# Performance work log

Measured on AMD Instinct MI355X. Metric: run time of the kernel, lower is better.

## Reference

```python
import jax, jax.numpy as jnp
import numpy as np
import math

B, S, D, H = 16, 1024, 512, 8
DK = D // H  # 64
EPS_T = 1e-06   # temperature epsilon
LN_EPS = 1e-05  # torch LayerNorm default


def gelu_tanh(x):
    return 0.5 * x * (1 + jnp.tanh(math.sqrt(2.0 / math.pi) * (x + 0.044715 * x ** 3)))


def layer_norm(x, g, b):
    mu = jnp.mean(x, axis=-1, keepdims=True)
    var = jnp.mean((x - mu) ** 2, axis=-1, keepdims=True)
    return (x - mu) * jax.lax.rsqrt(var + LN_EPS) * g + b


def setup_inputs() -> dict:
    key = jax.random.key(0)
    ks = jax.random.split(key, 12)
    std_qkv = np.sqrt(2.0 / (D + D)).astype(np.float32)
    inp = {
        "Q": jax.random.normal(ks[0], (B, S, D), jnp.float32),
        "K": jax.random.normal(ks[1], (B, S, D), jnp.float32),
        "V": jax.random.normal(ks[2], (B, S, D), jnp.float32),
        "mask": jnp.zeros((B, S), dtype=bool),  # no padding
        "W_q": jax.random.normal(ks[3], (D, D), jnp.float32) * std_qkv,
        "W_k": jax.random.normal(ks[4], (D, D), jnp.float32) * std_qkv,
        "W_v": jax.random.normal(ks[5], (D, D), jnp.float32) * std_qkv,
        "W_o": jax.random.normal(ks[6], (D, D), jnp.float32) * std_qkv,
        "lin1_w": jax.random.normal(ks[7], (D, D), jnp.float32) * std_qkv,  # stored [in,out]
        "lin1_b": jnp.zeros((D,), jnp.float32),
        "lin2_w": jax.random.normal(ks[8], (D, D), jnp.float32) * std_qkv,
        "lin2_b": jnp.zeros((D,), jnp.float32),
        "ln_g": jnp.ones((D,), jnp.float32),
        "ln_b": jnp.zeros((D,), jnp.float32),
    }
    return inp


def reference(Q, K, V, mask, W_q, W_k, W_v, W_o, lin1_w, lin1_b, lin2_w, lin2_b, ln_g, ln_b):
    b, q_len, _ = Q.shape
    # projections -> (b, h, s, d_k)
    Qh = (Q @ W_q).reshape(b, q_len, H, DK).transpose(0, 2, 1, 3)
    Kh = (K @ W_k).reshape(b, q_len, H, DK).transpose(0, 2, 1, 3)
    Vh = (V @ W_v).reshape(b, q_len, H, DK).transpose(0, 2, 1, 3)

    temperature = DK ** 0.5
    scores = jnp.einsum("bhqd,bhkd->bhqk", Qh, Kh) / (temperature + EPS_T)

    # mask: causal triu(diag=1) OR pad mask broadcast along k (as in original)
    causal = jnp.triu(jnp.ones((q_len, q_len), dtype=bool), k=1)  # (q,k)
    pad = mask[:, None, :, None]                                  # (b,1,q,1)
    mask_ = causal[None, None, :, :] | pad                        # (b,1,q,k)
    scores = jnp.where(mask_, -1e10, scores)

    attn = jax.nn.softmax(scores, axis=-1)
    ctx = jnp.einsum("bhqk,bhkd->bhqd", attn, Vh)
    ctx = ctx.transpose(0, 2, 1, 3).reshape(b, q_len, H * DK)
    v_att = ctx @ W_o  # dropout = identity (eval)

    out = layer_norm(Q + v_att, ln_g, ln_b)
    ffn = gelu_tanh(out @ lin1_w + lin1_b) @ lin2_w + lin2_b
    out = layer_norm(ffn + out, ln_g, ln_b)
    return out
```

## Files before the change

### kernel.cpp

```cpp
#include <hip/hip_runtime.h>
#include <cstdint>

using f32x4  = __attribute__((ext_vector_type(4))) float;
using f16x8  = __attribute__((ext_vector_type(8))) _Float16;
using f16x4  = __attribute__((ext_vector_type(4))) _Float16;
using f16x2  = __attribute__((ext_vector_type(2))) _Float16;

#define DEV static __device__ __forceinline__

DEV _Float16 f2h(float f) { return (_Float16)f; }

#if __has_builtin(__builtin_amdgcn_exp2f)
#define EXP2(x) __builtin_amdgcn_exp2f(x)
#else
#define EXP2(x) __expf((x) * 0.6931471805599453f)
#endif

DEV void gl2lds16(const void* g, void* l) {
  __builtin_amdgcn_global_load_lds(
      (__attribute__((address_space(1))) void*)(uintptr_t)g,
      (__attribute__((address_space(3))) void*)(uint32_t)(uintptr_t)l,
      16, 0, 0);
}

DEV f16x2 pack2(float a, float b) {
  return __builtin_bit_cast(f16x2, __builtin_amdgcn_cvt_pkrtz(a, b));
}

template <int MODE>
__global__ __launch_bounds__(256, 2) void gemm_k(
    const _Float16* __restrict__ A, const _Float16* __restrict__ Bt,
    const float* __restrict__ bias, _Float16* __restrict__ outB) {
  __shared__ _Float16 As[2][8192];
  __shared__ _Float16 Bs[2][8192];
  const int tid = threadIdx.x;
  const int lane = tid & 63, wv = tid >> 6;
  const int quad = lane >> 4, l16 = lane & 15;
  const int wm = wv & 1, wn = wv >> 1;

  const int bid = blockIdx.x;
  const int c8 = bid & 7, t8 = bid >> 3;
  const int nt = t8 & 3, gg = t8 >> 2;
  const int mz = gg * 8 + c8;
  const int m0 = (mz & 127) * 128;
  const int zz = (MODE == 0) ? (mz >> 7) : 0;
  const int n0 = nt * 128;

  const size_t zo = (size_t)zz * 8388608;
  const _Float16* Az = A + zo + (size_t)m0 * 512;
  const _Float16* Bz = Bt + (size_t)zz * 262144 + (size_t)n0 * 512;
  _Float16* Oz = outB + zo;

  f32x4 acc[4][4] = {};

  int aoff[4];
#pragma unroll
  for (int j = 0; j < 4; j++) {
    int e = j * 256 + tid;
    int r = e >> 3, c = e & 7;
    aoff[j] = r * 512 + (c ^ (r & 7)) * 8;
  }

  auto stage = [&](int kt, int pb) {
    const _Float16* Ab = Az + kt * 64;
    const _Float16* Bb = Bz + kt * 64;
#pragma unroll
    for (int j = 0; j < 4; j++)
      gl2lds16(Ab + aoff[j], &As[pb][(j * 256 + tid) * 8]);
#pragma unroll
    for (int j = 0; j < 4; j++)
      gl2lds16(Bb + aoff[j], &Bs[pb][(j * 256 + tid) * 8]);
  };

  stage(0, 0);
  __syncthreads();

  for (int kt = 0; kt < 8; kt++) {
    const int pb = kt & 1;
    if (kt < 7) stage(kt + 1, pb ^ 1);
    f16x8 af[2][4], bf[2][4];
#pragma unroll
    for (int kc = 0; kc < 2; kc++) {
#pragma unroll
      for (int i = 0; i < 4; i++) {
        int row = wm * 64 + i * 16 + l16;
        int q = (kc * 4 + quad) ^ (row & 7);
        af[kc][i] = *(const f16x8*)&As[pb][row * 64 + q * 8];
      }
#pragma unroll
      for (int j = 0; j < 4; j++) {
        int row = wn * 64 + j * 16 + l16;
        int q = (kc * 4 + quad) ^ (row & 7);
        bf[kc][j] = *(const f16x8*)&Bs[pb][row * 64 + q * 8];
      }
    }
#pragma unroll
    for (int kc = 0; kc < 2; kc++)
#pragma unroll
      for (int i = 0; i < 4; i++)
#pragma unroll
        for (int j = 0; j < 4; j++)
          acc[i][j] = __builtin_amdgcn_mfma_f32_16x16x32_f16(
              af[kc][i], bf[kc][j], acc[i][j], 0, 0, 0);
    __syncthreads();
  }

#pragma unroll
  for (int i = 0; i < 4; i++) {
#pragma unroll
    for (int j = 0; j < 4; j++) {
      const size_t col = n0 + wn * 64 + j * 16 + l16;
#pragma unroll
      for (int r = 0; r < 4; r++) {
        const size_t row = m0 + wm * 64 + i * 16 + quad * 4 + r;
        float v = acc[i][j][r];
        if (MODE == 0) {
          size_t b = row >> 10, s = row & 1023, h = col >> 6, d = col & 63;
          Oz[(((b * 8 + h) << 10) + s) * 64 + d] = f2h(v);
        } else if (MODE == 1) {
          Oz[row * 512 + col] = f2h(v);
        } else if (MODE == 2) {
          float x = v + bias[col];
          float u = 0.7978845608028654f * (x + 0.044715f * x * x * x);
          float t = __expf(2.f * u);
          float th = 1.f - 2.f / (t + 1.f);
          Oz[row * 512 + col] = f2h(0.5f * x * (1.f + th));
        } else {
          Oz[row * 512 + col] = f2h(v + bias[col]);
        }
      }
    }
  }
}

__global__ __launch_bounds__(256, 2) void attn_k(
    const _Float16* __restrict__ Qh, const _Float16* __restrict__ Kh,
    const _Float16* __restrict__ Vt, _Float16* __restrict__ ctx) {
  __shared__ _Float16 lds[16384];

  const int bid = blockIdx.x;
  const int pair = bid >> 7;
  const int bh = bid & 127;

  const _Float16* Qp = Qh + (size_t)bh * 65536;
  const _Float16* Kp = Kh + (size_t)bh * 65536;
  const _Float16* Vp = Vt + (size_t)bh * 65536;

  const int tid = threadIdx.x, lane = tid & 63, wv = tid >> 6;
  const int quad = lane >> 4, l16 = lane & 15;
  const int s7 = l16 & 7;
  const int b = bh >> 3, h = bh & 7;

  const int lin0 = 2 * wv * 64 + lane, lin1 = (2 * wv + 1) * 64 + lane;
  const int rK0 = lin0 >> 3, chK0 = (lane & 7) ^ (rK0 & 7);
  const int rK1 = lin1 >> 3, chK1 = (lane & 7) ^ (rK1 & 7);

  auto stage = [&](int kt, int pb) {
    _Float16* Kb = lds + pb * 4096;
    _Float16* Vb = lds + 8192 + pb * 4096;
    gl2lds16(Kp + (size_t)(kt * 64 + rK0) * 64 + chK0 * 8, Kb + lin0 * 8);
    gl2lds16(Kp + (size_t)(kt * 64 + rK1) * 64 + chK1 * 8, Kb + lin1 * 8);
    gl2lds16(Vp + (size_t)rK0 * 1024 + kt * 64 + chK0 * 8, Vb + lin0 * 8);
    gl2lds16(Vp + (size_t)rK1 * 1024 + kt * 64 + chK1 * 8, Vb + lin1 * 8);
  };

  const _Float16 qsc = f2h((1.0f / (8.0f + 1e-6f)) * 1.4426950408889634f);
  const f16x2 ones = {(_Float16)1.0f, (_Float16)1.0f};
  const float NEGM = -12.0f;

  for (int half = 0; half < 2; half++) {
    const int qblk = half ? (7 - pair) : pair;
    const int q0 = qblk * 128;
    const int ktmax = 2 * qblk + 1;
    const int wdiag = 2 * qblk + (wv >> 1);

    f16x8 bq[2][2];
#pragma unroll
    for (int qs = 0; qs < 2; qs++)
#pragma unroll
      for (int kc = 0; kc < 2; kc++) {
        f16x8 t = *(const f16x8*)&Qp[(size_t)(q0 + wv * 32 + qs * 16 + l16) *
                                         64 +
                                     kc * 32 + quad * 8];
#pragma unroll
        for (int r = 0; r < 8; r++) t[r] = t[r] * qsc;
        bq[qs][kc] = t;
      }
    int qg[2];
    qg[0] = q0 + wv * 32 + l16;
    qg[1] = qg[0] + 16;

    f32x4 ot[4][2] = {};
    float lrun[2] = {0.f, 0.f};

    stage(0, 0);
    __syncthreads();

    for (int kt = 0; kt <= ktmax; kt++) {
      if (kt < ktmax) stage(kt + 1, (kt + 1) & 1);

      if (kt <= wdiag) {
        const _Float16* Ks = lds + (kt & 1) * 4096;
        const _Float16* Vs = lds + 8192 + (kt & 1) * 4096;

        f32x4 sa[4][2];
#pragma unroll
        for (int ms = 0; ms < 4; ms++)
#pragma unroll
          for (int qs = 0; qs < 2; qs++)
            sa[ms][qs] = f32x4{NEGM, NEGM, NEGM, NEGM};

#pragma unroll
        for (int ms = 0; ms < 4; ms++) {
          const int row = ms * 16 + l16;
          const int sl0 = quad ^ s7;
          f16x8 ka0 = *(const f16x8*)&Ks[row * 64 + sl0 * 8];
          f16x8 ka1 = *(const f16x8*)&Ks[row * 64 + (sl0 ^ 4) * 8];
#pragma unroll
          for (int qs = 0; qs < 2; qs++) {
            sa[ms][qs] = __builtin_amdgcn_mfma_f32_16x16x32_f16(
                ka0, bq[qs][0], sa[ms][qs], 0, 0, 0);
            sa[ms][qs] = __builtin_amdgcn_mfma_f32_16x16x32_f16(
                ka1, bq[qs][1], sa[ms][qs], 0, 0, 0);
          }
        }

        if (kt == wdiag) {
#pragma unroll
          for (int ms = 0; ms < 4; ms++)
#pragma unroll
            for (int qs = 0; qs < 2; qs++)
#pragma unroll
              for (int r = 0; r < 4; r++) {
                int kg = kt * 64 + ms * 16 + quad * 4 + r;
                if (kg > qg[qs]) sa[ms][qs][r] = -3.0e38f;
              }
        }

        f16x4 pf[4][2];
#pragma unroll
        for (int ms = 0; ms < 4; ms++)
#pragma unroll
          for (int qs = 0; qs < 2; qs++) {
            float e0 = EXP2(sa[ms][qs][0]);
            float e1 = EXP2(sa[ms][qs][1]);
            float e2 = EXP2(sa[ms][qs][2]);
            float e3 = EXP2(sa[ms][qs][3]);
            f16x2 lo = pack2(e0, e1);
            f16x2 hi = pack2(e2, e3);
            lrun[qs] = __builtin_amdgcn_fdot2(lo, ones, lrun[qs], false);
            lrun[qs] = __builtin_amdgcn_fdot2(hi, ones, lrun[qs], false);
            f16x4 pk;
            pk[0] = lo[0]; pk[1] = lo[1]; pk[2] = hi[0]; pk[3] = hi[1];
            pf[ms][qs] = pk;
          }

#pragma unroll
        for (int ms = 0; ms < 4; ms++) {
          const int ch0 = (ms * 2 + (quad >> 1)) ^ s7;
#pragma unroll
          for (int ds = 0; ds < 4; ds++) {
            const int row = ds * 16 + l16;
            f16x4 vf =
                *(const f16x4*)&Vs[row * 64 + ch0 * 8 + (quad & 1) * 4];
#pragma unroll
            for (int qs = 0; qs < 2; qs++)
              ot[ds][qs] = __builtin_amdgcn_mfma_f32_16x16x16f16(
                  vf, pf[ms][qs], ot[ds][qs], 0, 0, 0);
          }
        }
      }
      __syncthreads();
    }

    float rinv[2];
#pragma unroll
    for (int qs = 0; qs < 2; qs++) {
      lrun[qs] += __shfl_xor(lrun[qs], 16, 64);
      lrun[qs] += __shfl_xor(lrun[qs], 32, 64);
      rinv[qs] = 1.0f / lrun[qs];
    }

    _Float16* Ol = lds + wv * 2176;
#pragma unroll
    for (int ds = 0; ds < 4; ds++)
#pragma unroll
      for (int qs = 0; qs < 2; qs++) {
        f16x4 pk;
#pragma unroll
        for (int r = 0; r < 4; r++) pk[r] = f2h(ot[ds][qs][r] * rinv[qs]);
        *(f16x4*)&Ol[(qs * 16 + l16) * 68 + ds * 16 + quad * 4] = pk;
      }
    __syncthreads();

#pragma unroll
    for (int rep = 0; rep < 4; rep++) {
      const int qq = rep * 8 + (lane >> 3);
      const int dc = lane & 7;
      f16x4 a = *(const f16x4*)&Ol[qq * 68 + dc * 8];
      f16x4 c = *(const f16x4*)&Ol[qq * 68 + dc * 8 + 4];
      f16x8 v;
      v[0] = a[0]; v[1] = a[1]; v[2] = a[2]; v[3] = a[3];
      v[4] = c[0]; v[5] = c[1]; v[6] = c[2]; v[7] = c[3];
      size_t row = (size_t)b * 1024 + q0 + wv * 32 + qq;
      *(f16x8*)&ctx[row * 512 + h * 64 + dc * 8] = v;
    }
    __syncthreads();
  }
}

__global__ void cast3_k(const float* __restrict__ Q, const float* __restrict__ K,
                        const float* __restrict__ V, _Float16* __restrict__ Qb,
                        _Float16* __restrict__ Kb, _Float16* __restrict__ Vb) {
  size_t i = (size_t)blockIdx.x * 256 + threadIdx.x;
  float4 q = ((const float4*)Q)[i];
  float4 k = ((const float4*)K)[i];
  float4 v = ((const float4*)V)[i];
  f16x4 o;
  o[0] = f2h(q.x); o[1] = f2h(q.y); o[2] = f2h(q.z); o[3] = f2h(q.w);
  ((f16x4*)Qb)[i] = o;
  o[0] = f2h(k.x); o[1] = f2h(k.y); o[2] = f2h(k.z); o[3] = f2h(k.w);
  ((f16x4*)Kb)[i] = o;
  o[0] = f2h(v.x); o[1] = f2h(v.y); o[2] = f2h(v.z); o[3] = f2h(v.w);
  ((f16x4*)Vb)[i] = o;
}

__global__ void wtrans_k(const float* W0, const float* W1, const float* W2,
                         const float* W3, const float* W4, const float* W5,
                         _Float16* dst) {
  __shared__ float t[32][33];
  const int z = blockIdx.z;
  const float* src = (z == 0) ? W0 : (z == 1) ? W1 : (z == 2) ? W2
                    : (z == 3) ? W3 : (z == 4) ? W4 : W5;
  _Float16* out = dst + (size_t)z * 262144;
  const int k0 = blockIdx.x * 32, n0 = blockIdx.y * 32;
  const int x = threadIdx.x, y = threadIdx.y;
  for (int j = y; j < 32; j += 8) t[j][x] = src[(size_t)(k0 + j) * 512 + n0 + x];
  __syncthreads();
  for (int j = y; j < 32; j += 8)
    out[(size_t)(n0 + j) * 512 + k0 + x] = f2h(t[x][j]);
}

__global__ void vtrans_k(const _Float16* __restrict__ Vh,
                         _Float16* __restrict__ Vt) {
  __shared__ _Float16 t[32][33];
  const int bh = blockIdx.z;
  const int s0 = blockIdx.x * 32, d0 = blockIdx.y * 32;
  const _Float16* src = Vh + (size_t)bh * 65536;
  _Float16* dst = Vt + (size_t)bh * 65536;
  const int x = threadIdx.x, y = threadIdx.y;
  for (int j = y; j < 32; j += 8) t[j][x] = src[(size_t)(s0 + j) * 64 + d0 + x];
  __syncthreads();
  for (int j = y; j < 32; j += 8)
    dst[(size_t)(d0 + j) * 1024 + s0 + x] = t[x][j];
}

template <bool F32OUT>
__global__ __launch_bounds__(128) void ln_k(
    const _Float16* __restrict__ X0, const _Float16* __restrict__ X1,
    const float* __restrict__ g, const float* __restrict__ bb,
    float* __restrict__ outF, _Float16* __restrict__ outB) {
  __shared__ float sh[4];
  const int row = blockIdx.x, t = threadIdx.x;
  const size_t base4 = (size_t)row * 128 + t;
  f16x4 a = ((const f16x4*)X0)[base4];
  f16x4 c = ((const f16x4*)X1)[base4];
  float x0 = (float)a[0] + (float)c[0];
  float x1 = (float)a[1] + (float)c[1];
  float x2 = (float)a[2] + (float)c[2];
  float x3 = (float)a[3] + (float)c[3];
  float s = x0 + x1 + x2 + x3;
  float ss = x0 * x0 + x1 * x1 + x2 * x2 + x3 * x3;
#pragma unroll
  for (int off = 1; off <= 32; off <<= 1) {
    s += __shfl_xor(s, off, 64);
    ss += __shfl_xor(ss, off, 64);
  }
  if ((t & 63) == 0) { sh[(t >> 6) * 2] = s; sh[(t >> 6) * 2 + 1] = ss; }
  __syncthreads();
  s = sh[0] + sh[2];
  ss = sh[1] + sh[3];
  const float mu = s * (1.f / 512.f);
  const float var = ss * (1.f / 512.f) - mu * mu;
  const float rstd = rsqrtf(var + 1e-5f);
  float4 gv = *(const float4*)(g + t * 4);
  float4 bv = *(const float4*)(bb + t * 4);
  float y0 = (x0 - mu) * rstd * gv.x + bv.x;
  float y1 = (x1 - mu) * rstd * gv.y + bv.y;
  float y2 = (x2 - mu) * rstd * gv.z + bv.z;
  float y3 = (x3 - mu) * rstd * gv.w + bv.w;
  if (F32OUT) {
    float4 o; o.x = y0; o.y = y1; o.z = y2; o.w = y3;
    *(float4*)(outF + (size_t)row * 512 + t * 4) = o;
  } else {
    f16x4 ob; ob[0] = f2h(y0); ob[1] = f2h(y1); ob[2] = f2h(y2); ob[3] = f2h(y3);
    ((f16x4*)outB)[base4] = ob;
  }
}

extern "C" void kernel_launch(void* const* d_in, const int* in_sizes, int n_in,
                              void* d_out, int out_size, void* d_ws,
                              size_t ws_size, hipStream_t stream) {
  const float* Q = (const float*)d_in[0];
  const float* K = (const float*)d_in[1];
  const float* V = (const float*)d_in[2];
  const float* Wq = (const float*)d_in[4];
  const float* Wk = (const float*)d_in[5];
  const float* Wv = (const float*)d_in[6];
  const float* Wo = (const float*)d_in[7];
  const float* l1w = (const float*)d_in[8];
  const float* l1b = (const float*)d_in[9];
  const float* l2w = (const float*)d_in[10];
  const float* l2b = (const float*)d_in[11];
  const float* lng = (const float*)d_in[12];
  const float* lnb = (const float*)d_in[13];
  float* out = (float*)d_out;

  uint8_t* w = (uint8_t*)d_ws;
  const size_t MB = 1ull << 20;
  _Float16* Qb = (_Float16*)(w + 0);
  _Float16* Kb = (_Float16*)(w + 16 * MB);
  _Float16* Vb = (_Float16*)(w + 32 * MB);
  _Float16* Wt = (_Float16*)(w + 48 * MB);
  _Float16* Qh = (_Float16*)(w + 52 * MB);
  _Float16* Kh = (_Float16*)(w + 68 * MB);
  _Float16* VhN = (_Float16*)(w + 84 * MB);
  _Float16* Vt = (_Float16*)(w + 100 * MB);
  _Float16* ctx = VhN;
  _Float16* vatt = Vt;
  _Float16* h1 = Kb;
  _Float16* out1h = Vb;
  _Float16* f2b = Qh;

  cast3_k<<<8192, 256, 0, stream>>>(Q, K, V, Qb, Kb, Vb);
  wtrans_k<<<dim3(16, 16, 6), dim3(32, 8), 0, stream>>>(Wq, Wk, Wv, Wo, l1w,
                                                        l2w, Wt);
  gemm_k<0><<<1536, 256, 0, stream>>>(Qb, Wt, nullptr, Qh);
  vtrans_k<<<dim3(32, 2, 128), dim3(32, 8), 0, stream>>>(VhN, Vt);
  attn_k<<<512, 256, 0, stream>>>(Qh, Kh, Vt, ctx);
  gemm_k<1><<<512, 256, 0, stream>>>(ctx, Wt + 3 * 262144, nullptr, vatt);
  ln_k<false><<<16384, 128, 0, stream>>>(Qb, vatt, lng, lnb, nullptr, out1h);
  gemm_k<2><<<512, 256, 0, stream>>>(out1h, Wt + 4 * 262144, l1b, h1);
  gemm_k<3><<<512, 256, 0, stream>>>(h1, Wt + 5 * 262144, l2b, f2b);
  ln_k<true><<<16384, 128, 0, stream>>>(f2b, out1h, lng, lnb, out, nullptr);
}
```

Before: 294.5 us.

## Fuse fp32-to-fp16 input cast into QKV GEMM and vectorize GEMM stores

Removes the separate cast kernel. The QKV projection GEMM now loads fp32 Q/K/V directly, converts them to fp16 in registers and writes them into LDS. The MFMA operands are swapped so each lane holds four consecutive columns, which allows 4-wide fp16 stores in the epilogue instead of scalar stores. The first LayerNorm reads the fp32 Q residual directly, which also improves residual precision. In exchange, the A-tile loads no longer use the asynchronous global-to-LDS path, so they go through registers and may overlap less with compute.

```diff
diff --git a/kernel.cpp b/kernel.cpp
--- a/kernel.cpp
+++ b/kernel.cpp
@@ -29,10 +29,10 @@
 
 template <int MODE>
 __global__ __launch_bounds__(256, 2) void gemm_k(
-    const _Float16* __restrict__ A, const _Float16* __restrict__ Bt,
+    const void* __restrict__ A0, const void* __restrict__ A1,
+    const void* __restrict__ A2, const _Float16* __restrict__ Bt,
     const float* __restrict__ bias, _Float16* __restrict__ outB) {
-  __shared__ _Float16 As[2][8192];
-  __shared__ _Float16 Bs[2][8192];
+  __shared__ _Float16 smem[32768];
   const int tid = threadIdx.x;
   const int lane = tid & 63, wv = tid >> 6;
   const int quad = lane >> 4, l16 = lane & 15;
@@ -46,10 +46,17 @@
   const int zz = (MODE == 0) ? (mz >> 7) : 0;
   const int n0 = nt * 128;
 
-  const size_t zo = (size_t)zz * 8388608;
-  const _Float16* Az = A + zo + (size_t)m0 * 512;
+  const float* Az32 = nullptr;
+  const _Float16* Az16 = nullptr;
+  if (MODE == 0) {
+    const float* base = (zz == 0) ? (const float*)A0
+                        : (zz == 1) ? (const float*)A1 : (const float*)A2;
+    Az32 = base + (size_t)m0 * 512;
+  } else {
+    Az16 = (const _Float16*)A0 + (size_t)m0 * 512;
+  }
   const _Float16* Bz = Bt + (size_t)zz * 262144 + (size_t)n0 * 512;
-  _Float16* Oz = outB + zo;
+  _Float16* Oz = outB + (size_t)zz * 8388608;
 
   f32x4 acc[4][4] = {};
 
@@ -62,14 +69,32 @@
   }
 
   auto stage = [&](int kt, int pb) {
-    const _Float16* Ab = Az + kt * 64;
+    _Float16* As = smem + pb * 8192;
+    _Float16* Bs = smem + 16384 + pb * 8192;
+    if (MODE == 0) {
+      const float* Af = Az32 + kt * 64;
+#pragma unroll
+      for (int j = 0; j < 4; j++) {
+        const float* src = Af + aoff[j];
+        float4 v0 = *(const float4*)src;
+        float4 v1 = *(const float4*)(src + 4);
+        f16x2 p0 = pack2(v0.x, v0.y), p1 = pack2(v0.z, v0.w);
+        f16x2 p2 = pack2(v1.x, v1.y), p3 = pack2(v1.z, v1.w);
+        f16x8 pk;
+        pk[0] = p0[0]; pk[1] = p0[1]; pk[2] = p1[0]; pk[3] = p1[1];
+        pk[4] = p2[0]; pk[5] = p2[1]; pk[6] = p3[0]; pk[7] = p3[1];
+        *(f16x8*)&As[(j * 256 + tid) * 8] = pk;
+      }
+    } else {
+      const _Float16* Af = Az16 + kt * 64;
+#pragma unroll
+      for (int j = 0; j < 4; j++)
+        gl2lds16(Af + aoff[j], &As[(j * 256 + tid) * 8]);
+    }
     const _Float16* Bb = Bz + kt * 64;
 #pragma unroll
     for (int j = 0; j < 4; j++)
-      gl2lds16(Ab + aoff[j], &As[pb][(j * 256 + tid) * 8]);
-#pragma unroll
-    for (int j = 0; j < 4; j++)
-      gl2lds16(Bb + aoff[j], &Bs[pb][(j * 256 + tid) * 8]);
+      gl2lds16(Bb + aoff[j], &Bs[(j * 256 + tid) * 8]);
   };
 
   stage(0, 0);
@@ -78,6 +103,8 @@
   for (int kt = 0; kt < 8; kt++) {
     const int pb = kt & 1;
     if (kt < 7) stage(kt + 1, pb ^ 1);
+    const _Float16* As = smem + pb * 8192;
+    const _Float16* Bs = smem + 16384 + pb * 8192;
     f16x8 af[2][4], bf[2][4];
 #pragma unroll
     for (int kc = 0; kc < 2; kc++) {
@@ -85,13 +112,13 @@
       for (int i = 0; i < 4; i++) {
         int row = wm * 64 + i * 16 + l16;
         int q = (kc * 4 + quad) ^ (row & 7);
-        af[kc][i] = *(const f16x8*)&As[pb][row * 64 + q * 8];
+        af[kc][i] = *(const f16x8*)&As[row * 64 + q * 8];
       }
 #pragma unroll
       for (int j = 0; j < 4; j++) {
         int row = wn * 64 + j * 16 + l16;
         int q = (kc * 4 + quad) ^ (row & 7);
-        bf[kc][j] = *(const f16x8*)&Bs[pb][row * 64 + q * 8];
+        bf[kc][j] = *(const f16x8*)&Bs[row * 64 + q * 8];
       }
     }
 #pragma unroll
@@ -101,33 +128,39 @@
 #pragma unroll
         for (int j = 0; j < 4; j++)
           acc[i][j] = __builtin_amdgcn_mfma_f32_16x16x32_f16(
-              af[kc][i], bf[kc][j], acc[i][j], 0, 0, 0);
+              bf[kc][j], af[kc][i], acc[i][j], 0, 0, 0);
     __syncthreads();
   }
 
 #pragma unroll
   for (int i = 0; i < 4; i++) {
+    const size_t row = m0 + wm * 64 + i * 16 + l16;
 #pragma unroll
     for (int j = 0; j < 4; j++) {
-      const size_t col = n0 + wn * 64 + j * 16 + l16;
-#pragma unroll
-      for (int r = 0; r < 4; r++) {
-        const size_t row = m0 + wm * 64 + i * 16 + quad * 4 + r;
-        float v = acc[i][j][r];
-        if (MODE == 0) {
-          size_t b = row >> 10, s = row & 1023, h = col >> 6, d = col & 63;
-          Oz[(((b * 8 + h) << 10) + s) * 64 + d] = f2h(v);
-        } else if (MODE == 1) {
-          Oz[row * 512 + col] = f2h(v);
-        } else if (MODE == 2) {
-          float x = v + bias[col];
+      const int colb = n0 + wn * 64 + j * 16 + quad * 4;
+      f16x4 o;
+      if (MODE == 2) {
+#pragma unroll
+        for (int r = 0; r < 4; r++) {
+          float x = acc[i][j][r] + bias[colb + r];
           float u = 0.7978845608028654f * (x + 0.044715f * x * x * x);
           float t = __expf(2.f * u);
           float th = 1.f - 2.f / (t + 1.f);
-          Oz[row * 512 + col] = f2h(0.5f * x * (1.f + th));
-        } else {
-          Oz[row * 512 + col] = f2h(v + bias[col]);
+          o[r] = f2h(0.5f * x * (1.f + th));
         }
+      } else if (MODE == 3) {
+#pragma unroll
+        for (int r = 0; r < 4; r++) o[r] = f2h(acc[i][j][r] + bias[colb + r]);
+      } else {
+#pragma unroll
+        for (int r = 0; r < 4; r++) o[r] = f2h(acc[i][j][r]);
+      }
+      if (MODE == 0) {
+        size_t b = row >> 10, s = row & 1023;
+        size_t h = colb >> 6, d = colb & 63;
+        *(f16x4*)&Oz[(((b * 8 + h) << 10) + s) * 64 + d] = o;
+      } else {
+        *(f16x4*)&Oz[row * 512 + colb] = o;
       }
     }
   }
@@ -307,22 +340,6 @@
     }
     __syncthreads();
   }
-}
-
-__global__ void cast3_k(const float* __restrict__ Q, const float* __restrict__ K,
-                        const float* __restrict__ V, _Float16* __restrict__ Qb,
-                        _Float16* __restrict__ Kb, _Float16* __restrict__ Vb) {
-  size_t i = (size_t)blockIdx.x * 256 + threadIdx.x;
-  float4 q = ((const float4*)Q)[i];
-  float4 k = ((const float4*)K)[i];
-  float4 v = ((const float4*)V)[i];
-  f16x4 o;
-  o[0] = f2h(q.x); o[1] = f2h(q.y); o[2] = f2h(q.z); o[3] = f2h(q.w);
-  ((f16x4*)Qb)[i] = o;
-  o[0] = f2h(k.x); o[1] = f2h(k.y); o[2] = f2h(k.z); o[3] = f2h(k.w);
-  ((f16x4*)Kb)[i] = o;
-  o[0] = f2h(v.x); o[1] = f2h(v.y); o[2] = f2h(v.z); o[3] = f2h(v.w);
-  ((f16x4*)Vb)[i] = o;
 }
 
 __global__ void wtrans_k(const float* W0, const float* W1, const float* W2,
@@ -355,20 +372,24 @@
     dst[(size_t)(d0 + j) * 1024 + s0 + x] = t[x][j];
 }
 
-template <bool F32OUT>
+template <bool RES32, bool F32OUT>
 __global__ __launch_bounds__(128) void ln_k(
-    const _Float16* __restrict__ X0, const _Float16* __restrict__ X1,
+    const void* __restrict__ X0, const _Float16* __restrict__ X1,
     const float* __restrict__ g, const float* __restrict__ bb,
     float* __restrict__ outF, _Float16* __restrict__ outB) {
   __shared__ float sh[4];
   const int row = blockIdx.x, t = threadIdx.x;
   const size_t base4 = (size_t)row * 128 + t;
-  f16x4 a = ((const f16x4*)X0)[base4];
+  float x0, x1, x2, x3;
+  if (RES32) {
+    float4 a = ((const float4*)X0)[base4];
+    x0 = a.x; x1 = a.y; x2 = a.z; x3 = a.w;
+  } else {
+    f16x4 a = ((const f16x4*)X0)[base4];
+    x0 = (float)a[0]; x1 = (float)a[1]; x2 = (float)a[2]; x3 = (float)a[3];
+  }
   f16x4 c = ((const f16x4*)X1)[base4];
-  float x0 = (float)a[0] + (float)c[0];
-  float x1 = (float)a[1] + (float)c[1];
-  float x2 = (float)a[2] + (float)c[2];
-  float x3 = (float)a[3] + (float)c[3];
+  x0 += (float)c[0]; x1 += (float)c[1]; x2 += (float)c[2]; x3 += (float)c[3];
   float s = x0 + x1 + x2 + x3;
   float ss = x0 * x0 + x1 * x1 + x2 * x2 + x3 * x3;
 #pragma unroll
@@ -418,29 +439,30 @@
 
   uint8_t* w = (uint8_t*)d_ws;
   const size_t MB = 1ull << 20;
-  _Float16* Qb = (_Float16*)(w + 0);
-  _Float16* Kb = (_Float16*)(w + 16 * MB);
-  _Float16* Vb = (_Float16*)(w + 32 * MB);
-  _Float16* Wt = (_Float16*)(w + 48 * MB);
-  _Float16* Qh = (_Float16*)(w + 52 * MB);
-  _Float16* Kh = (_Float16*)(w + 68 * MB);
-  _Float16* VhN = (_Float16*)(w + 84 * MB);
-  _Float16* Vt = (_Float16*)(w + 100 * MB);
+  _Float16* Wt = (_Float16*)(w + 0);
+  _Float16* Qh = (_Float16*)(w + 4 * MB);
+  _Float16* Kh = (_Float16*)(w + 20 * MB);
+  _Float16* VhN = (_Float16*)(w + 36 * MB);
+  _Float16* Vt = (_Float16*)(w + 52 * MB);
+  _Float16* h1 = (_Float16*)(w + 68 * MB);
+  _Float16* out1h = (_Float16*)(w + 84 * MB);
   _Float16* ctx = VhN;
   _Float16* vatt = Vt;
-  _Float16* h1 = Kb;
-  _Float16* out1h = Vb;
   _Float16* f2b = Qh;
 
-  cast3_k<<<8192, 256, 0, stream>>>(Q, K, V, Qb, Kb, Vb);
   wtrans_k<<<dim3(16, 16, 6), dim3(32, 8), 0, stream>>>(Wq, Wk, Wv, Wo, l1w,
                                                         l2w, Wt);
-  gemm_k<0><<<1536, 256, 0, stream>>>(Qb, Wt, nullptr, Qh);
+  gemm_k<0><<<1536, 256, 0, stream>>>(Q, K, V, Wt, nullptr, Qh);
   vtrans_k<<<dim3(32, 2, 128), dim3(32, 8), 0, stream>>>(VhN, Vt);
   attn_k<<<512, 256, 0, stream>>>(Qh, Kh, Vt, ctx);
-  gemm_k<1><<<512, 256, 0, stream>>>(ctx, Wt + 3 * 262144, nullptr, vatt);
-  ln_k<false><<<16384, 128, 0, stream>>>(Qb, vatt, lng, lnb, nullptr, out1h);
-  gemm_k<2><<<512, 256, 0, stream>>>(out1h, Wt + 4 * 262144, l1b, h1);
-  gemm_k<3><<<512, 256, 0, stream>>>(h1, Wt + 5 * 262144, l2b, f2b);
-  ln_k<true><<<16384, 128, 0, stream>>>(f2b, out1h, lng, lnb, out, nullptr);
-}
+  gemm_k<1><<<512, 256, 0, stream>>>(ctx, nullptr, nullptr, Wt + 3 * 262144,
+                                     nullptr, vatt);
+  ln_k<true, false><<<16384, 128, 0, stream>>>(Q, vatt, lng, lnb, nullptr,
+                                               out1h);
+  gemm_k<2><<<512, 256, 0, stream>>>(out1h, nullptr, nullptr, Wt + 4 * 262144,
+                                     l1b, h1);
+  gemm_k<3><<<512, 256, 0, stream>>>(h1, nullptr, nullptr, Wt + 5 * 262144,
+                                     l2b, f2b);
+  ln_k<false, true><<<16384, 128, 0, stream>>>(f2b, out1h, lng, lnb, out,
+                                               nullptr);
+}
```

After: 317.9 us. +7.9%, slower.
